# Kernel tuning notes

Measured on AMD Instinct MI355X. Metric: run time of the kernel, lower is better.

The kernel has to match this reference:

```python
import jax, jax.numpy as jnp
import numpy as np

N_CODES = 8192
EMBED_DIM = 64
N_VOXELS = 32768


def setup_inputs() -> dict:
    key = jax.random.key(0)
    k1, k2 = jax.random.split(key)
    z_feats = jax.random.normal(k1, (N_VOXELS, EMBED_DIM), dtype=jnp.float32)
    embeddings = jax.random.normal(k2, (N_CODES, EMBED_DIM), dtype=jnp.float32)
    return {"z_feats": z_feats, "embeddings": embeddings}


def reference(z_feats, embeddings):
    # Pairwise squared euclidean distances: ||z||^2 - 2 z.e + ||e||^2  [N, K]
    z_sq = jnp.sum(z_feats * z_feats, axis=1, keepdims=True)        # [N, 1]
    e_sq = jnp.sum(embeddings * embeddings, axis=1)[None, :]        # [1, K]
    d2 = z_sq - 2.0 * jnp.einsum('nd,kd->nk', z_feats, embeddings) + e_sq
    # argmin is invariant under sqrt (cdist returns sqrt, but only indices are used)
    encoding_indices = jnp.argmin(d2, axis=1)                        # [N]
    quantized_feats = embeddings[encoding_indices]                   # [N, D]
    # commitment_loss = mse(z, sg(q));  vq_loss = mse(q, sg(z)) (gradient mode)
    commitment_loss = jnp.mean((z_feats - jax.lax.stop_gradient(quantized_feats)) ** 2)
    vq_loss = jnp.mean((quantized_feats - jax.lax.stop_gradient(z_feats)) ** 2)
    # straight-through estimator
    quantized_st = z_feats + jax.lax.stop_gradient(quantized_feats - z_feats)
    indices_out = encoding_indices[:, None].astype(jnp.float32)      # [N, 1]
    return quantized_st, vq_loss, commitment_loss, indices_out
```

## Files before the change

### kernel.cpp

```cpp
#include <hip/hip_runtime.h>
#include <float.h>

#define N_VOX 32768
#define N_CODES 8192
#define DIM 64

#define Q_OFF 0
#define VQ_OFF (N_VOX * DIM)
#define CM_OFF (VQ_OFF + 1)
#define IDX_OFF (VQ_OFF + 2)

#define WS_ACC 0
#define WS_CNT 1
#define WS_ESQH 64
#define WS_IDX (WS_ESQH + N_CODES)
#define WS_EHI (WS_IDX + N_VOX)
#define WS_ELO (WS_EHI + N_CODES * DIM / 2)

typedef _Float16 half8 __attribute__((ext_vector_type(8)));
typedef float floatx4 __attribute__((ext_vector_type(4)));

__device__ inline void gld16(const void* g, void* l) {
  __builtin_amdgcn_global_load_lds(
      (const __attribute__((address_space(1))) unsigned int*)g,
      (__attribute__((address_space(3))) unsigned int*)l, 16, 0, 0);
}
__device__ inline void gld4(const void* g, void* l) {
  __builtin_amdgcn_global_load_lds(
      (const __attribute__((address_space(1))) unsigned int*)g,
      (__attribute__((address_space(3))) unsigned int*)l, 4, 0, 0);
}

__device__ __forceinline__ floatx4 mfma16(half8 a, half8 b, floatx4 c) {
  return __builtin_amdgcn_mfma_f32_16x16x32_f16(a, b, c, 0, 0, 0);
}

__global__ __launch_bounds__(256) void k_cvt(const float* __restrict__ e,
                                             float* __restrict__ ws) {
  int gid = blockIdx.x * 256 + threadIdx.x;
  if (gid == 0) {
    ws[WS_ACC] = 0.f;
    ((int*)ws)[WS_CNT] = 0;
  }
  int row = gid >> 3, c = gid & 7;
  const float* src = e + (size_t)row * DIM + c * 8;
  float4 a = *(const float4*)src;
  float4 b = *(const float4*)(src + 4);
  float x[8] = {a.x, a.y, a.z, a.w, b.x, b.y, b.z, b.w};
  float s = 0.f;
  half8 hv, lv;
  #pragma unroll
  for (int j = 0; j < 8; ++j) {
    s += x[j] * x[j];
    _Float16 h = (_Float16)x[j];
    hv[j] = h;
    lv[j] = (_Float16)(x[j] - (float)h);
  }
  s += __shfl_xor(s, 1); s += __shfl_xor(s, 2); s += __shfl_xor(s, 4);
  if (c == 0) ws[WS_ESQH + row] = -0.5f * s;
  int p = (c + row) & 7;
  ((half8*)(ws + WS_EHI))[row * 8 + p] = hv;
  ((half8*)(ws + WS_ELO))[row * 8 + p] = lv;
}

__global__ __launch_bounds__(256, 2) void k_argmin(const float* __restrict__ z,
                                                   const float* __restrict__ e,
                                                   float* __restrict__ ws,
                                                   float* __restrict__ out) {
  __shared__ __align__(16) _Float16 sBhi[2][128 * 64];
  __shared__ __align__(16) _Float16 sBlo[2][128 * 64];
  __shared__ float sEsq[2][128];
  __shared__ float sMval[4][64];
  __shared__ int   sMidx[4][64];
  __shared__ int   sWin[64];
  __shared__ float sWsum[4];

  const int tid  = threadIdx.x;
  const int lane = tid & 63;
  const int wave = tid >> 6;
  const int n16  = lane & 15;
  const int quad = lane >> 4;
  const int vb = blockIdx.x * 64;

  const char* ehi_b = (const char*)(ws + WS_EHI);
  const char* elo_b = (const char*)(ws + WS_ELO);
  const char* esq_b = (const char*)(ws + WS_ESQH);

  half8 ahi[4][2], alo[4][2];
  #pragma unroll
  for (int m = 0; m < 4; ++m)
    #pragma unroll
    for (int kc = 0; kc < 2; ++kc) {
      const float* src = z + (size_t)(vb + m * 16 + n16) * DIM
                       + kc * 32 + quad * 8;
      float4 a = *(const float4*)src;
      float4 b = *(const float4*)(src + 4);
      float x[8] = {a.x, a.y, a.z, a.w, b.x, b.y, b.z, b.w};
      #pragma unroll
      for (int j = 0; j < 8; ++j) {
        _Float16 h = (_Float16)x[j];
        ahi[m][kc][j] = h;
        alo[m][kc][j] = (_Float16)(x[j] - (float)h);
      }
    }

  float bmax[4][4]; int bidx[4][4];
  #pragma unroll
  for (int m = 0; m < 4; ++m)
    #pragma unroll
    for (int r = 0; r < 4; ++r) { bmax[m][r] = -FLT_MAX; bidx[m][r] = 0; }

  const int s0 = ((quad + n16) & 7) * 8;
  const int s1 = ((quad + 4 + n16) & 7) * 8;

  auto stage = [&](int buf, int ct) {
    const size_t cbb = (size_t)ct * 128 * 128;
    #pragma unroll
    for (int r = 0; r < 4; ++r) {
      int off = (r * 4 + wave) * 1024;
      gld16(ehi_b + cbb + off + lane * 16, (char*)sBhi[buf] + off);
      gld16(elo_b + cbb + off + lane * 16, (char*)sBlo[buf] + off);
    }
    if (wave == 0) {
      gld4(esq_b + (size_t)ct * 512 + lane * 4, (char*)sEsq[buf]);
      gld4(esq_b + (size_t)ct * 512 + 256 + lane * 4, (char*)sEsq[buf] + 256);
    }
  };

  stage(0, 0);
  __syncthreads();

  for (int ct = 0; ct < 64; ++ct) {
    const int cur = ct & 1;
    if (ct < 63) stage(cur ^ 1, ct + 1);

    const _Float16* bhiP = sBhi[cur];
    const _Float16* bloP = sBlo[cur];
    const float*    esqP = sEsq[cur];
    const int cbase = ct * 128;

    #pragma unroll
    for (int t = 0; t < 2; ++t) {
      const int row = wave * 32 + t * 16 + n16;
      half8 bh0 = *(const half8*)&bhiP[row * 64 + s0];
      half8 bh1 = *(const half8*)&bhiP[row * 64 + s1];
      half8 bl0 = *(const half8*)&bloP[row * 64 + s0];
      half8 bl1 = *(const half8*)&bloP[row * 64 + s1];
      float nh = esqP[row];
      int code = cbase + row;
      __builtin_amdgcn_s_setprio(1);
      #pragma unroll
      for (int m = 0; m < 4; ++m) {
        floatx4 acc0 = {nh, nh, nh, nh};
        floatx4 acc1 = {0.f, 0.f, 0.f, 0.f};
        acc0 = mfma16(ahi[m][0], bh0, acc0);
        acc1 = mfma16(ahi[m][1], bh1, acc1);
        acc0 = mfma16(ahi[m][0], bl0, acc0);
        acc1 = mfma16(ahi[m][1], bl1, acc1);
        acc0 = mfma16(alo[m][0], bh0, acc0);
        acc1 = mfma16(alo[m][1], bh1, acc1);
        #pragma unroll
        for (int r = 0; r < 4; ++r) {
          float tv = acc0[r] + acc1[r];
          if (tv > bmax[m][r]) { bmax[m][r] = tv; bidx[m][r] = code; }
        }
      }
      __builtin_amdgcn_s_setprio(0);
    }
    __syncthreads();
  }

  #pragma unroll
  for (int m = 0; m < 4; ++m)
    #pragma unroll
    for (int r = 0; r < 4; ++r) {
      float v = bmax[m][r]; int i = bidx[m][r];
      #pragma unroll
      for (int off = 1; off < 16; off <<= 1) {
        float ov = __shfl_xor(v, off);
        int   oi = __shfl_xor(i, off);
        if (ov > v || (ov == v && oi < i)) { v = ov; i = oi; }
      }
      if (n16 == 0) {
        sMval[wave][m * 16 + quad * 4 + r] = v;
        sMidx[wave][m * 16 + quad * 4 + r] = i;
      }
    }
  __syncthreads();

  if (tid < 64) {
    float v = sMval[0][tid]; int i = sMidx[0][tid];
    #pragma unroll
    for (int q = 1; q < 4; ++q) {
      float ov = sMval[q][tid]; int oi = sMidx[q][tid];
      if (ov > v || (ov == v && oi < i)) { v = ov; i = oi; }
    }
    sWin[tid] = i;
    out[IDX_OFF + vb + tid] = (float)i;
  }
  __syncthreads();

  {
    const int vox = tid >> 2;
    const int dc = (tid & 3) * 16;
    const int gi = sWin[vox];
    const float* er = e + (size_t)gi * DIM + dc;
    const float* zr = z + (size_t)(vb + vox) * DIM + dc;
    float* qr = out + Q_OFF + (size_t)(vb + vox) * DIM + dc;
    float local = 0.f;
    #pragma unroll
    for (int j = 0; j < 4; ++j) {
      float4 e4 = *(const float4*)(er + j * 4);
      float4 z4 = *(const float4*)(zr + j * 4);
      *(float4*)(qr + j * 4) = e4;
      float dx = z4.x - e4.x, dy = z4.y - e4.y, dz = z4.z - e4.z, dw = z4.w - e4.w;
      local += dx * dx + dy * dy + dz * dz + dw * dw;
    }
    #pragma unroll
    for (int off = 32; off; off >>= 1) local += __shfl_xor(local, off);
    if ((tid & 63) == 0) sWsum[wave] = local;
    __syncthreads();
    if (tid == 0) {
      float bs = sWsum[0] + sWsum[1] + sWsum[2] + sWsum[3];
      atomicAdd(ws + WS_ACC, bs);
      __threadfence();
      int done = atomicAdd((int*)ws + WS_CNT, 1);
      if (done == (int)gridDim.x - 1) {
        float s = atomicAdd(ws + WS_ACC, 0.f);
        float mv = s * (1.0f / (float)(N_VOX * DIM));
        out[VQ_OFF] = mv;
        out[CM_OFF] = mv;
      }
    }
  }
}

extern "C" void kernel_launch(void* const* d_in, const int* in_sizes, int n_in,
                              void* d_out, int out_size, void* d_ws, size_t ws_size,
                              hipStream_t stream) {
  const float* z = (const float*)d_in[0];
  const float* e = (const float*)d_in[1];
  float* out = (float*)d_out;
  float* ws = (float*)d_ws;

  k_cvt<<<(N_CODES * 8) / 256, 256, 0, stream>>>(e, ws);
  k_argmin<<<N_VOX / 64, 256, 0, stream>>>(z, e, ws, out);
}
```

Baseline: 199.7 us.

## Give each wave a private codebook slice and remove block barriers from the loop

```diff
diff --git a/kernel.cpp b/kernel.cpp
--- a/kernel.cpp
+++ b/kernel.cpp
@@ -24,11 +24,6 @@
   __builtin_amdgcn_global_load_lds(
       (const __attribute__((address_space(1))) unsigned int*)g,
       (__attribute__((address_space(3))) unsigned int*)l, 16, 0, 0);
-}
-__device__ inline void gld4(const void* g, void* l) {
-  __builtin_amdgcn_global_load_lds(
-      (const __attribute__((address_space(1))) unsigned int*)g,
-      (__attribute__((address_space(3))) unsigned int*)l, 4, 0, 0);
 }
 
 __device__ __forceinline__ floatx4 mfma16(half8 a, half8 b, floatx4 c) {
@@ -67,9 +62,7 @@
                                                    const float* __restrict__ e,
                                                    float* __restrict__ ws,
                                                    float* __restrict__ out) {
-  __shared__ __align__(16) _Float16 sBhi[2][128 * 64];
-  __shared__ __align__(16) _Float16 sBlo[2][128 * 64];
-  __shared__ float sEsq[2][128];
+  __shared__ __align__(16) _Float16 sB[4][2][2][2048];
   __shared__ float sMval[4][64];
   __shared__ int   sMidx[4][64];
   __shared__ int   sWin[64];
@@ -81,10 +74,11 @@
   const int n16  = lane & 15;
   const int quad = lane >> 4;
   const int vb = blockIdx.x * 64;
+  const int wcode = wave * 2048;
 
   const char* ehi_b = (const char*)(ws + WS_EHI);
   const char* elo_b = (const char*)(ws + WS_ELO);
-  const char* esq_b = (const char*)(ws + WS_ESQH);
+  const float* esqG = ws + WS_ESQH + wcode;
 
   half8 ahi[4][2], alo[4][2];
   #pragma unroll
@@ -103,6 +97,7 @@
         alo[m][kc][j] = (_Float16)(x[j] - (float)h);
       }
     }
+  __builtin_amdgcn_sched_barrier(0);
 
   float bmax[4][4]; int bidx[4][4];
   #pragma unroll
@@ -113,62 +108,79 @@
   const int s0 = ((quad + n16) & 7) * 8;
   const int s1 = ((quad + 4 + n16) & 7) * 8;
 
-  auto stage = [&](int buf, int ct) {
-    const size_t cbb = (size_t)ct * 128 * 128;
+  auto stagew = [&](int buf, int ct) {
+    const size_t gb = (size_t)(wcode + ct * 32) * 128;
+    char* dH = (char*)&sB[wave][buf][0][0];
+    char* dL = (char*)&sB[wave][buf][1][0];
     #pragma unroll
     for (int r = 0; r < 4; ++r) {
-      int off = (r * 4 + wave) * 1024;
-      gld16(ehi_b + cbb + off + lane * 16, (char*)sBhi[buf] + off);
-      gld16(elo_b + cbb + off + lane * 16, (char*)sBlo[buf] + off);
-    }
-    if (wave == 0) {
-      gld4(esq_b + (size_t)ct * 512 + lane * 4, (char*)sEsq[buf]);
-      gld4(esq_b + (size_t)ct * 512 + 256 + lane * 4, (char*)sEsq[buf] + 256);
+      gld16(ehi_b + gb + r * 1024 + lane * 16, dH + r * 1024);
+      gld16(elo_b + gb + r * 1024 + lane * 16, dL + r * 1024);
     }
   };
 
-  stage(0, 0);
-  __syncthreads();
-
-  for (int ct = 0; ct < 64; ++ct) {
-    const int cur = ct & 1;
-    if (ct < 63) stage(cur ^ 1, ct + 1);
-
-    const _Float16* bhiP = sBhi[cur];
-    const _Float16* bloP = sBlo[cur];
-    const float*    esqP = sEsq[cur];
-    const int cbase = ct * 128;
-
-    #pragma unroll
-    for (int t = 0; t < 2; ++t) {
-      const int row = wave * 32 + t * 16 + n16;
-      half8 bh0 = *(const half8*)&bhiP[row * 64 + s0];
-      half8 bh1 = *(const half8*)&bhiP[row * 64 + s1];
-      half8 bl0 = *(const half8*)&bloP[row * 64 + s0];
-      half8 bl1 = *(const half8*)&bloP[row * 64 + s1];
-      float nh = esqP[row];
-      int code = cbase + row;
-      __builtin_amdgcn_s_setprio(1);
-      #pragma unroll
-      for (int m = 0; m < 4; ++m) {
-        floatx4 acc0 = {nh, nh, nh, nh};
-        floatx4 acc1 = {0.f, 0.f, 0.f, 0.f};
-        acc0 = mfma16(ahi[m][0], bh0, acc0);
-        acc1 = mfma16(ahi[m][1], bh1, acc1);
-        acc0 = mfma16(ahi[m][0], bl0, acc0);
-        acc1 = mfma16(ahi[m][1], bl1, acc1);
-        acc0 = mfma16(alo[m][0], bh0, acc0);
-        acc1 = mfma16(alo[m][1], bh1, acc1);
-        #pragma unroll
-        for (int r = 0; r < 4; ++r) {
-          float tv = acc0[r] + acc1[r];
-          if (tv > bmax[m][r]) { bmax[m][r] = tv; bidx[m][r] = code; }
-        }
-      }
-      __builtin_amdgcn_s_setprio(0);
-    }
-    __syncthreads();
-  }
+  stagew(0, 0);
+  __builtin_amdgcn_sched_barrier(0);
+  float nqA0 = esqG[n16];
+  float nqA1 = esqG[16 + n16];
+  __builtin_amdgcn_sched_barrier(0);
+  stagew(1, 1);
+  __builtin_amdgcn_sched_barrier(0);
+  float nqB0 = 0.f, nqB1 = 0.f;
+
+#define ITER(CT, CUR, NQ0, NQ1, NQN0, NQN1)                                   \
+  {                                                                           \
+    if ((CT) < 63) { asm volatile("s_waitcnt vmcnt(10)" ::: "memory"); }      \
+    else           { asm volatile("s_waitcnt vmcnt(2)"  ::: "memory"); }      \
+    __builtin_amdgcn_sched_barrier(0);                                        \
+    const _Float16* bp = &sB[wave][CUR][0][0];                                \
+    const _Float16* lp = &sB[wave][CUR][1][0];                                \
+    half8 bh00 = *(const half8*)&bp[n16 * 64 + s0];                           \
+    half8 bh01 = *(const half8*)&bp[n16 * 64 + s1];                           \
+    half8 bh10 = *(const half8*)&bp[(16 + n16) * 64 + s0];                    \
+    half8 bh11 = *(const half8*)&bp[(16 + n16) * 64 + s1];                    \
+    half8 bl00 = *(const half8*)&lp[n16 * 64 + s0];                           \
+    half8 bl01 = *(const half8*)&lp[n16 * 64 + s1];                           \
+    half8 bl10 = *(const half8*)&lp[(16 + n16) * 64 + s0];                    \
+    half8 bl11 = *(const half8*)&lp[(16 + n16) * 64 + s1];                    \
+    if ((CT) + 1 < 64) {                                                      \
+      NQN0 = esqG[((CT) + 1) * 32 + n16];                                     \
+      NQN1 = esqG[((CT) + 1) * 32 + 16 + n16];                                \
+    }                                                                         \
+    asm volatile("s_waitcnt lgkmcnt(0)" ::: "memory");                        \
+    __builtin_amdgcn_sched_barrier(0);                                        \
+    if ((CT) + 2 < 64) stagew(CUR, (CT) + 2);                                 \
+    __builtin_amdgcn_sched_barrier(0);                                        \
+    const int code0 = wcode + (CT) * 32 + n16;                                \
+    __builtin_amdgcn_s_setprio(1);                                            \
+    _Pragma("unroll")                                                         \
+    for (int m = 0; m < 4; ++m) {                                             \
+      floatx4 a0 = {0.f, 0.f, 0.f, 0.f};                                      \
+      floatx4 a1 = {0.f, 0.f, 0.f, 0.f};                                      \
+      a0 = mfma16(ahi[m][0], bh00, a0);  a1 = mfma16(ahi[m][1], bh01, a1);    \
+      a0 = mfma16(ahi[m][0], bl00, a0);  a1 = mfma16(ahi[m][1], bl01, a1);    \
+      a0 = mfma16(alo[m][0], bh00, a0);  a1 = mfma16(alo[m][1], bh01, a1);    \
+      floatx4 c0 = {0.f, 0.f, 0.f, 0.f};                                      \
+      floatx4 c1 = {0.f, 0.f, 0.f, 0.f};                                      \
+      c0 = mfma16(ahi[m][0], bh10, c0);  c1 = mfma16(ahi[m][1], bh11, c1);    \
+      c0 = mfma16(ahi[m][0], bl10, c0);  c1 = mfma16(ahi[m][1], bl11, c1);    \
+      c0 = mfma16(alo[m][0], bh10, c0);  c1 = mfma16(alo[m][1], bh11, c1);    \
+      _Pragma("unroll")                                                       \
+      for (int r = 0; r < 4; ++r) {                                           \
+        float t0 = a0[r] + a1[r] + (NQ0);                                     \
+        float t1 = c0[r] + c1[r] + (NQ1);                                     \
+        if (t0 > bmax[m][r]) { bmax[m][r] = t0; bidx[m][r] = code0; }         \
+        if (t1 > bmax[m][r]) { bmax[m][r] = t1; bidx[m][r] = code0 + 16; }    \
+      }                                                                       \
+    }                                                                         \
+    __builtin_amdgcn_s_setprio(0);                                            \
+  }
+
+  for (int ct2 = 0; ct2 < 64; ct2 += 2) {
+    ITER(ct2,     0, nqA0, nqA1, nqB0, nqB1);
+    ITER(ct2 + 1, 1, nqB0, nqB1, nqA0, nqA1);
+  }
+#undef ITER
 
   #pragma unroll
   for (int m = 0; m < 4; ++m)
```

New measurement: 189.6 us. 1.05x faster.
